# Optimization experiments

Measured on AMD Instinct MI355X. Metric: run time of the kernel, lower is better.

## Reference

```python
import jax, jax.numpy as jnp
import numpy as np

B, T, D, H, DEPTH, FF, NC = 512, 150, 256, 8, 6, 1024, 4
HD = D // H  # head dim = 32


def setup_inputs() -> dict:
    key = jax.random.key(0)
    ks = iter(jax.random.split(key, 64))
    n = lambda shape, s=0.02: jax.random.normal(next(ks), shape, jnp.float32) * s
    return dict(
        token_types=jax.random.randint(next(ks), (B, T), 0, 4, jnp.int32),
        decision_ids=jax.random.randint(next(ks), (B, T), 0, NC, jnp.int32),
        action_vals=jax.random.normal(next(ks), (B, T, 1), jnp.float32),
        dis_vals=jax.random.normal(next(ks), (B, T, 10), jnp.float32),
        v_vals=jax.random.normal(next(ks), (B, T, 3), jnp.float32),
        action_W=n((1, D), 0.5), action_b=n((D,)),
        dis_W=n((10, D), 0.2), dis_b=n((D,)),
        v_W=n((3, D), 0.3), v_b=n((D,)),
        decision_table=n((NC, D)),
        pos_embed=n((1, T + 1, D)), cls_token=n((1, 1, D)),
        qkv_W=n((DEPTH, D, 3 * D), 0.05), qkv_b=jnp.zeros((DEPTH, 3 * D), jnp.float32),
        out_W=n((DEPTH, D, D), 0.05), out_b=jnp.zeros((DEPTH, D), jnp.float32),
        ln1_g=jnp.ones((DEPTH, D), jnp.float32), ln1_b=jnp.zeros((DEPTH, D), jnp.float32),
        ln2_g=jnp.ones((DEPTH, D), jnp.float32), ln2_b=jnp.zeros((DEPTH, D), jnp.float32),
        ffn1_W=n((DEPTH, D, FF), 0.05), ffn1_b=jnp.zeros((DEPTH, FF), jnp.float32),
        ffn2_W=n((DEPTH, FF, D), 0.05), ffn2_b=jnp.zeros((DEPTH, D), jnp.float32),
        dec_ln_g=jnp.ones((D,), jnp.float32), dec_ln_b=jnp.zeros((D,), jnp.float32),
        dec_W=n((D, NC), 0.05), dec_b=jnp.zeros((NC,), jnp.float32),
        act_ln_g=jnp.ones((D,), jnp.float32), act_ln_b=jnp.zeros((D,), jnp.float32),
        act_W=n((D, 1), 0.05), act_b=jnpp if False else jnp.zeros((1,), jnp.float32),
    )


def _ln(x, g, b):
    # PyTorch LayerNorm: eps=1e-5, biased variance
    m = jnp.mean(x, axis=-1, keepdims=True)
    v = jnp.mean(jnp.square(x - m), axis=-1, keepdims=True)
    return (x - m) * jax.lax.rsqrt(v + 1e-5) * g + b


def reference(token_types, decision_ids, action_vals, dis_vals, v_vals,
              action_W, action_b, dis_W, dis_b, v_W, v_b, decision_table,
              pos_embed, cls_token, qkv_W, qkv_b, out_W, out_b,
              ln1_g, ln1_b, ln2_g, ln2_b, ffn1_W, ffn1_b, ffn2_W, ffn2_b,
              dec_ln_g, dec_ln_b, dec_W, dec_b, act_ln_g, act_ln_b, act_W, act_b):
    # --- batched type-dispatched token embedding (replaces the per-token python loop) ---
    a_emb = action_vals @ action_W + action_b                     # [B,T,D] type 'A'
    s_emb = dis_vals @ dis_W + dis_b + v_vals @ v_W + v_b         # [B,T,D] type 'S'
    d_emb = decision_table[decision_ids]                          # [B,T,D] type 'D'
    t = token_types[..., None]
    x = jnp.where(t == 0, a_emb, jnp.where(t == 1, s_emb, jnp.where(t == 2, d_emb, 0.0)))
    # --- prepend CLS, add positional embedding ---
    x = jnp.concatenate([jnp.broadcast_to(cls_token, (x.shape[0], 1, D)), x], axis=1)
    S = x.shape[1]
    x = x + pos_embed[:, :S, :]
    # --- post-norm TransformerEncoder (PyTorch default: ReLU FFN, norm_first=False, eval/no dropout) ---
    scale = 1.0 / np.sqrt(HD).astype(np.float32)
    for i in range(DEPTH):
        qkv = x @ qkv_W[i] + qkv_b[i]                             # [B,S,3D]
        q, k, v = jnp.split(qkv, 3, axis=-1)
        q = q.reshape(-1, S, H, HD)
        k = k.reshape(-1, S, H, HD)
        v = v.reshape(-1, S, H, HD)
        att = jax.nn.softmax(jnp.einsum('bqhd,bkhd->bhqk', q, k) * scale, axis=-1)
        o = jnp.einsum('bhqk,bkhd->bqhd', att, v).reshape(-1, S, D)
        x = _ln(x + o @ out_W[i] + out_b[i], ln1_g[i], ln1_b[i])
        ff = jax.nn.relu(x @ ffn1_W[i] + ffn1_b[i]) @ ffn2_W[i] + ffn2_b[i]
        x = _ln(x + ff, ln2_g[i], ln2_b[i])
    cls = x[:, 0, :]
    decision_logits = _ln(cls, dec_ln_g, dec_ln_b) @ dec_W + dec_b   # [B,4]
    action_pred = _ln(cls, act_ln_g, act_ln_b) @ act_W + act_b       # [B,1]
    return (decision_logits, action_pred)
```

## Files before the change

kernel.cpp:

```cpp
#include <hip/hip_runtime.h>
#include <hip/hip_bf16.h>

typedef __hip_bfloat16 bf16;
typedef unsigned short u16;
typedef __attribute__((ext_vector_type(8))) short s16x8;
typedef __attribute__((ext_vector_type(4))) float f32x4;

#define B_ 512
#define T_ 150
#define S_ 151
#define D_ 256
#define H_ 8
#define HD_ 32
#define FF_ 1024
#define NC_ 4
#define DEPTH_ 6
#define MTOT 77312
#define MT128 (MTOT / 128)
#define MT64 (MTOT / 64)

#define XOFF 0
#define C1OFF (MTOT * D_)
#define C2OFF (C1OFF + MTOT * FF_)
#define WSELEMS (C2OFF + MTOT * D_)

#define QKVT_OFF 0
#define OUTT_OFF (QKVT_OFF + DEPTH_ * D_ * 768)
#define FFN1T_OFF (OUTT_OFF + DEPTH_ * D_ * D_)
#define FFN2T_OFF (FFN1T_OFF + DEPTH_ * D_ * FF_)
#define WTELEMS (FFN2T_OFF + DEPTH_ * FF_ * D_)

__device__ __align__(16) u16 g_ws[WSELEMS];
__device__ __align__(16) u16 g_wt[WTELEMS];
__device__ int g_f32flag;

__device__ __forceinline__ float ldf(const void* p, size_t i, int f) {
  return f ? ((const float*)p)[i] : __bfloat162float(((const bf16*)p)[i]);
}
__device__ __forceinline__ float b2f(u16 u) {
  union { unsigned int i; float f; } v; v.i = ((unsigned int)u) << 16; return v.f;
}
__device__ __forceinline__ u16 f2b(float x) {
  bf16 h = __float2bfloat16(x);
  return *reinterpret_cast<u16*>(&h);
}

typedef __attribute__((address_space(3))) void lds_void;
typedef const __attribute__((address_space(1))) void glob_void;
__device__ __forceinline__ void gload_lds16(const u16* g, u16* l) {
  __builtin_amdgcn_global_load_lds((glob_void*)g, (lds_void*)l, 16, 0, 0);
}

#define PROBE_N 38656
__global__ __launch_bounds__(256) void probe_kernel(const void* pe)
{
  const u16* w = (const u16*)pe;
  int susp = 0, zeroEven = 0;
  for (int k = threadIdx.x; k < PROBE_N; k += 256) {
    u16 u = w[k];
    int ex = (u >> 7) & 0xFF;
    if (ex >= 141) susp++;
    if ((k & 1) == 0 && (u & 0x7FFF) == 0) zeroEven++;
  }
  __shared__ int s_susp, s_zero;
  if (threadIdx.x == 0) { s_susp = 0; s_zero = 0; }
  __syncthreads();
  atomicAdd(&s_susp, susp);
  atomicAdd(&s_zero, zeroEven);
  __syncthreads();
  if (threadIdx.x == 0)
    g_f32flag = (s_susp > 0 || s_zero >= ((PROBE_N / 2) * 9) / 10) ? 1 : 0;
}

__global__ __launch_bounds__(256) void wtrans_kernel(const void* src, int dstOff,
                                                     int K, int N, int total)
{
  const int f = g_f32flag;
  int idx = blockIdx.x * 256 + threadIdx.x;
  if (idx >= total) return;
  int kn = K * N;
  int l = idx / kn;
  int r = idx - l * kn;
  int k = r / N;
  int n = r - k * N;
  g_wt[dstOff + (size_t)l * kn + (size_t)n * K + k] = f2b(ldf(src, idx, f));
}

__global__ __launch_bounds__(256) void embed_kernel(
    const int* __restrict__ tt, const int* __restrict__ dids,
    const void* av, const void* dv, const void* vv,
    const void* aW, const void* ab, const void* dW, const void* db,
    const void* vW, const void* vb, const void* table, const void* pos,
    const void* cls)
{
  const int f = g_f32flag;
  u16* x = g_ws + XOFF;
  int row = blockIdx.x;
  int d = threadIdx.x;
  int b = row / S_;
  int s = row - b * S_;
  float val;
  if (s == 0) {
    val = ldf(cls, d, f);
  } else {
    int t = s - 1;
    int idx = b * T_ + t;
    int ty = tt[idx];
    if (ty == 0) {
      val = ldf(av, idx, f) * ldf(aW, d, f) + ldf(ab, d, f);
    } else if (ty == 1) {
      float acc = ldf(db, d, f) + ldf(vb, d, f);
#pragma unroll
      for (int i = 0; i < 10; i++) acc += ldf(dv, (size_t)idx * 10 + i, f) * ldf(dW, i * D_ + d, f);
#pragma unroll
      for (int i = 0; i < 3; i++) acc += ldf(vv, (size_t)idx * 3 + i, f) * ldf(vW, i * D_ + d, f);
      val = acc;
    } else if (ty == 2) {
      int did = dids[idx] & (NC_ - 1);
      val = ldf(table, (size_t)did * D_ + d, f);
    } else {
      val = 0.f;
    }
  }
  val += ldf(pos, s * D_ + d, f);
  x[(size_t)row * D_ + d] = f2b(val);
}

__global__ __launch_bounds__(256, 3) void gemm_mfma(
    int aOff, int wtOff, const void* bias, size_t bOff,
    int cOff, int N, int K, int relu, int NB)
{
  const int f = g_f32flag;
  const u16* A = g_ws + aOff;
  const u16* Bt = g_wt + wtOff;
  u16* C = g_ws + cOff;
  __shared__ __align__(16) u16 sm[16384];
  const int tid = threadIdx.x;

  int gblk = blockIdx.x;
  int bm, bn;
  {
    const int full = (MT128 / 8) * 8;
    if (gblk < NB * full) {
      int per = NB * 8;
      int grp = gblk / per, rem = gblk % per;
      bm = grp * 8 + (rem & 7);
      bn = rem >> 3;
    } else {
      int id = gblk - NB * full;
      bm = full + id / NB;
      bn = id % NB;
    }
  }

  const int lane = tid & 63, wid = tid >> 6;
  const int wm = (wid >> 1) * 64, wn = (wid & 1) * 64;
  const int frow = lane & 15, quad = lane >> 4;

  const int rg = lane >> 3;
  const int ck = ((lane & 7) ^ rg) * 8;
  const u16* Ag[4]; const u16* Bg[4];
  u16 *Asl[4], *Bsl[4];
#pragma unroll
  for (int p = 0; p < 4; p++) {
    int grp = wid * 4 + p;
    int row = grp * 8 + rg;
    Ag[p] = A + (size_t)(bm * 128 + row) * K + ck;
    Bg[p] = Bt + (size_t)(bn * 128 + row) * K + ck;
    Asl[p] = &sm[grp * 512];
    Bsl[p] = &sm[8192 + grp * 512];
  }

  f32x4 acc[4][4] = {};

  for (int kt = 0; kt < K; kt += 64) {
    if (kt) __syncthreads();
#pragma unroll
    for (int p = 0; p < 4; p++) {
      gload_lds16(Ag[p] + kt, Asl[p]);
      gload_lds16(Bg[p] + kt, Bsl[p]);
    }
    __syncthreads();
#pragma unroll
    for (int s = 0; s < 2; s++) {
      s16x8 af[4], bfr[4];
      const int cfr = ((s * 4 + quad) ^ (frow & 7)) * 8;
#pragma unroll
      for (int t = 0; t < 4; t++) {
        af[t]  = *(const s16x8*)&sm[(wm + t * 16 + frow) * 64 + cfr];
        bfr[t] = *(const s16x8*)&sm[8192 + (wn + t * 16 + frow) * 64 + cfr];
      }
#pragma unroll
      for (int mt = 0; mt < 4; mt++)
#pragma unroll
        for (int nt = 0; nt < 4; nt++)
          acc[mt][nt] = __builtin_amdgcn_mfma_f32_16x16x32_bf16(af[mt], bfr[nt], acc[mt][nt], 0, 0, 0);
    }
  }

  float bv[4];
#pragma unroll
  for (int nt = 0; nt < 4; nt++)
    bv[nt] = ldf(bias, bOff + (size_t)(bn * 128 + wn + nt * 16 + frow), f);
  __syncthreads();
#pragma unroll
  for (int p = 0; p < 2; p++) {
    if ((wid >> 1) == p) {
#pragma unroll
      for (int mt = 0; mt < 4; mt++)
#pragma unroll
        for (int nt = 0; nt < 4; nt++)
#pragma unroll
          for (int r = 0; r < 4; r++) {
            int rl = (wm & 63) + mt * 16 + quad * 4 + r;
            float v = acc[mt][nt][r] + bv[nt];
            if (relu) v = fmaxf(v, 0.f);
            sm[rl * 136 + wn + nt * 16 + frow] = f2b(v);
          }
    }
    __syncthreads();
    {
      int rl = tid >> 2;
      int cq = (tid & 3) * 32;
      size_t gb = (size_t)(bm * 128 + p * 64 + rl) * N + bn * 128 + cq;
#pragma unroll
      for (int j = 0; j < 4; j++)
        *(s16x8*)(C + gb + j * 8) = *(const s16x8*)&sm[rl * 136 + cq + j * 8];
    }
    __syncthreads();
  }
}

__global__ __launch_bounds__(256, 4) void gemm_ln(
    int aOff, int wtOff, const void* bias, size_t bOff,
    const void* lng, const void* lnb, size_t lnOff, int K)
{
  const int f = g_f32flag;
  const u16* A = g_ws + aOff;
  const u16* Bt = g_wt + wtOff;
  __shared__ __align__(16) u16 sm[20480];
  const int tid = threadIdx.x;
  const int bm = blockIdx.x;
  const int lane = tid & 63, wid = tid >> 6;
  const int wn = wid * 64;
  const int frow = lane & 15, quad = lane >> 4;
  const int rg = lane >> 3;
  const int ck = ((lane & 7) ^ rg) * 8;

  const u16* Ag[2]; u16* Asl[2];
  const u16* Bg[8]; u16* Bsl[8];
#pragma unroll
  for (int p = 0; p < 2; p++) {
    int grp = wid * 2 + p;
    Ag[p] = A + (size_t)(bm * 64 + grp * 8 + rg) * K + ck;
    Asl[p] = &sm[grp * 512];
  }
#pragma unroll
  for (int p = 0; p < 8; p++) {
    int grp = wid * 8 + p;
    Bg[p] = Bt + (size_t)(grp * 8 + rg) * K + ck;
    Bsl[p] = &sm[4096 + grp * 512];
  }

  f32x4 acc[4][4] = {};

  for (int kt = 0; kt < K; kt += 64) {
    if (kt) __syncthreads();
#pragma unroll
    for (int p = 0; p < 2; p++) gload_lds16(Ag[p] + kt, Asl[p]);
#pragma unroll
    for (int p = 0; p < 8; p++) gload_lds16(Bg[p] + kt, Bsl[p]);
    __syncthreads();
#pragma unroll
    for (int s = 0; s < 2; s++) {
      s16x8 af[4], bfr[4];
      const int cfr = ((s * 4 + quad) ^ (frow & 7)) * 8;
#pragma unroll
      for (int t = 0; t < 4; t++) {
        af[t]  = *(const s16x8*)&sm[(t * 16 + frow) * 64 + cfr];
        bfr[t] = *(const s16x8*)&sm[4096 + (wn + t * 16 + frow) * 64 + cfr];
      }
#pragma unroll
      for (int mt = 0; mt < 4; mt++)
#pragma unroll
        for (int nt = 0; nt < 4; nt++)
          acc[mt][nt] = __builtin_amdgcn_mfma_f32_16x16x32_bf16(af[mt], bfr[nt], acc[mt][nt], 0, 0, 0);
    }
  }

  float bv[4];
#pragma unroll
  for (int nt = 0; nt < 4; nt++)
    bv[nt] = ldf(bias, bOff + (size_t)(wn + nt * 16 + frow), f);
  __syncthreads();
#pragma unroll
  for (int mt = 0; mt < 4; mt++)
#pragma unroll
    for (int nt = 0; nt < 4; nt++)
#pragma unroll
      for (int r = 0; r < 4; r++) {
        int row = mt * 16 + quad * 4 + r;
        int col = wn + nt * 16 + frow;
        sm[row * 264 + col] = f2b(acc[mt][nt][r] + bv[nt]);
      }
  __syncthreads();
  {
    int rl = tid >> 2;
    int cq = (tid & 3) * 64;
    size_t rowg = (size_t)bm * 64 + rl;
    float s1 = 0.f, s2 = 0.f;
#pragma unroll
    for (int j = 0; j < 8; j++) {
      s16x8 yv = *(const s16x8*)&sm[rl * 264 + cq + j * 8];
      s16x8 xv = *(const s16x8*)(g_ws + XOFF + rowg * 256 + cq + j * 8);
#pragma unroll
      for (int e = 0; e < 8; e++) {
        float v = b2f((u16)yv[e]) + b2f((u16)xv[e]);
        s1 += v; s2 += v * v;
      }
    }
    s1 += __shfl_xor(s1, 1, 64); s2 += __shfl_xor(s2, 1, 64);
    s1 += __shfl_xor(s1, 2, 64); s2 += __shfl_xor(s2, 2, 64);
    float mean = s1 * (1.f / 256.f);
    float var = s2 * (1.f / 256.f) - mean * mean;
    float rs = rsqrtf(var + 1e-5f);
#pragma unroll
    for (int j = 0; j < 8; j++) {
      s16x8 yv = *(const s16x8*)&sm[rl * 264 + cq + j * 8];
      s16x8 xv = *(const s16x8*)(g_ws + XOFF + rowg * 256 + cq + j * 8);
      s16x8 ov;
#pragma unroll
      for (int e = 0; e < 8; e++) {
        float v = b2f((u16)yv[e]) + b2f((u16)xv[e]);
        int col = cq + j * 8 + e;
        ov[e] = (short)f2b((v - mean) * rs * ldf(lng, lnOff + col, f) + ldf(lnb, lnOff + col, f));
      }
      *(s16x8*)(g_ws + XOFF + rowg * 256 + cq + j * 8) = ov;
    }
  }
}

#define SP 160
#define KLD 32
#define VLD 170
#define PLDS 42

__global__ __launch_bounds__(320) void attn_kernel()
{
  const u16* qkv = g_ws + C1OFF;
  u16* o = g_ws + C2OFF;
  __shared__ __align__(16) u16 Ks[SP * KLD];
  __shared__ __align__(16) u16 Vt[HD_ * VLD];
  __shared__ __align__(16) u16 Ps[5][16 * PLDS];
  int bh = blockIdx.x;
  int b = bh >> 3, h = bh & 7;
  int tid = threadIdx.x;
  int lane = tid & 63, wid = tid >> 6;
  const u16* base = qkv + (size_t)b * S_ * 768;

  {
    const int jrow = lane >> 2;
    const int dsw = (((lane & 3) ^ ((lane >> 3) & 3)) * 8);
#pragma unroll
    for (int p = 0; p < 2; p++) {
      int g = wid * 2 + p;
      int j = g * 16 + jrow;
      gload_lds16(base + (size_t)j * 768 + 256 + h * 32 + dsw, &Ks[g * 512]);
    }
  }
  for (int g = tid; g < SP * 4; g += 320) {
    int j = g >> 2, d0 = (g & 3) * 8;
    s16x8 vv = {0, 0, 0, 0, 0, 0, 0, 0};
    if (j < S_) vv = *(const s16x8*)(base + (size_t)j * 768 + 512 + h * 32 + d0);
#pragma unroll
    for (int i = 0; i < 8; i++) Vt[(d0 + i) * VLD + j] = (u16)vv[i];
  }
  __syncthreads();

  const int frow = lane & 15;
  const int quad = lane >> 4;
  const int fk = quad * 8;
  const float scale = 0.17677669529663687f;
  u16* Pw = &Ps[wid][0];

  for (int round = 0; round < 2; round++) {
    int mt = round * 5 + wid;
    int qrow = mt * 16 + frow;
    s16x8 aq = {0, 0, 0, 0, 0, 0, 0, 0};
    if (qrow < S_) aq = *(const s16x8*)(base + (size_t)qrow * 768 + h * 32 + fk);
    f32x4 sacc[10];
#pragma unroll
    for (int nt = 0; nt < 10; nt++) {
      s16x8 bk = *(const s16x8*)&Ks[(nt * 16 + frow) * KLD
                                    + ((quad ^ ((frow >> 1) & 3)) * 8)];
      f32x4 z = {0.f, 0.f, 0.f, 0.f};
      sacc[nt] = __builtin_amdgcn_mfma_f32_16x16x32_bf16(aq, bk, z, 0, 0, 0);
    }
#pragma unroll
    for (int nt = 0; nt < 10; nt++) {
      int colg = nt * 16 + frow;
      float msk = (colg < S_) ? 1.f : 0.f;
#pragma unroll
      for (int r = 0; r < 4; r++)
        sacc[nt][r] = msk ? sacc[nt][r] * scale : -1e30f;
    }
    float inv[4];
#pragma unroll
    for (int r = 0; r < 4; r++) {
      float mx = -1e30f;
#pragma unroll
      for (int nt = 0; nt < 10; nt++) mx = fmaxf(mx, sacc[nt][r]);
#pragma unroll
      for (int m = 1; m < 16; m <<= 1) mx = fmaxf(mx, __shfl_xor(mx, m, 64));
      float sm2 = 0.f;
#pragma unroll
      for (int nt = 0; nt < 10; nt++) {
        float p = __expf(sacc[nt][r] - mx);
        sacc[nt][r] = p;
        sm2 += p;
      }
#pragma unroll
      for (int m = 1; m < 16; m <<= 1) sm2 += __shfl_xor(sm2, m, 64);
      inv[r] = 1.f / sm2;
    }
    f32x4 oacc[2] = {};
#pragma unroll
    for (int ks = 0; ks < 5; ks++) {
#pragma unroll
      for (int h2 = 0; h2 < 2; h2++) {
        int nt = ks * 2 + h2;
#pragma unroll
        for (int r = 0; r < 4; r++)
          Pw[(quad * 4 + r) * PLDS + h2 * 16 + frow] = f2b(sacc[nt][r]);
      }
      s16x8 ap = *(const s16x8*)&Pw[frow * PLDS + fk];
#pragma unroll
      for (int nt2 = 0; nt2 < 2; nt2++) {
        s16x8 bv = *(const s16x8*)&Vt[(nt2 * 16 + frow) * VLD + ks * 32 + fk];
        oacc[nt2] = __builtin_amdgcn_mfma_f32_16x16x32_bf16(ap, bv, oacc[nt2], 0, 0, 0);
      }
    }
#pragma unroll
    for (int nt2 = 0; nt2 < 2; nt2++)
#pragma unroll
      for (int r = 0; r < 4; r++) {
        int rowg = mt * 16 + quad * 4 + r;
        if (rowg < S_)
          o[(size_t)(b * S_ + rowg) * D_ + h * 32 + nt2 * 16 + frow] = f2b(oacc[nt2][r] * inv[r]);
      }
  }
}

__global__ __launch_bounds__(256) void head_kernel(
    const void* dg, const void* dbt, const void* dW, const void* dbias,
    const void* ag, const void* abt, const void* aW, const void* abias,
    void* out)
{
  const int f = g_f32flag;
  const u16* x = g_ws + XOFF;
  int bg = blockIdx.x;
  int tid = threadIdx.x;
  float c = b2f(x[(size_t)bg * S_ * D_ + tid]);
  float s1 = c, s2 = c * c;
#pragma unroll
  for (int off = 32; off > 0; off >>= 1) {
    s1 += __shfl_down(s1, off, 64);
    s2 += __shfl_down(s2, off, 64);
  }
  __shared__ float ws1[4], ws2[4], stats[2];
  __shared__ float lnD[256], lnA[256];
  int wid = tid >> 6, lane = tid & 63;
  if (lane == 0) { ws1[wid] = s1; ws2[wid] = s2; }
  __syncthreads();
  if (tid == 0) {
    float t1 = ws1[0] + ws1[1] + ws1[2] + ws1[3];
    float t2 = ws2[0] + ws2[1] + ws2[2] + ws2[3];
    float mean = t1 * (1.f / 256.f);
    float var = t2 * (1.f / 256.f) - mean * mean;
    stats[0] = mean;
    stats[1] = rsqrtf(var + 1e-5f);
  }
  __syncthreads();
  float n = (c - stats[0]) * stats[1];
  lnD[tid] = n * ldf(dg, tid, f) + ldf(dbt, tid, f);
  lnA[tid] = n * ldf(ag, tid, f) + ldf(abt, tid, f);
  __syncthreads();
  if (tid < NC_) {
    float acc = ldf(dbias, tid, f);
    for (int k = 0; k < D_; k++) acc += lnD[k] * ldf(dW, k * NC_ + tid, f);
    if (f) ((float*)out)[bg * NC_ + tid] = acc;
    else   ((bf16*)out)[bg * NC_ + tid] = __float2bfloat16(acc);
  } else if (tid == 8) {
    float acc = ldf(abias, 0, f);
    for (int k = 0; k < D_; k++) acc += lnA[k] * ldf(aW, k, f);
    if (f) ((float*)out)[B_ * NC_ + bg] = acc;
    else   ((bf16*)out)[B_ * NC_ + bg] = __float2bfloat16(acc);
  }
}

extern "C" void kernel_launch(void* const* d_in, const int* in_sizes, int n_in,
                              void* d_out, int out_size, void* d_ws, size_t ws_size,
                              hipStream_t stream)
{
  (void)in_sizes; (void)out_size; (void)d_ws; (void)ws_size;
  if (n_in < 34) return;
  const int* token_types  = (const int*)d_in[0];
  const int* decision_ids = (const int*)d_in[1];

  probe_kernel<<<1, 256, 0, stream>>>(d_in[12]);

  wtrans_kernel<<<(DEPTH_ * D_ * 768 + 255) / 256, 256, 0, stream>>>(
      d_in[14], QKVT_OFF, D_, 768, DEPTH_ * D_ * 768);
  wtrans_kernel<<<(DEPTH_ * D_ * D_ + 255) / 256, 256, 0, stream>>>(
      d_in[16], OUTT_OFF, D_, D_, DEPTH_ * D_ * D_);
  wtrans_kernel<<<(DEPTH_ * D_ * FF_ + 255) / 256, 256, 0, stream>>>(
      d_in[22], FFN1T_OFF, D_, FF_, DEPTH_ * D_ * FF_);
  wtrans_kernel<<<(DEPTH_ * FF_ * D_ + 255) / 256, 256, 0, stream>>>(
      d_in[24], FFN2T_OFF, FF_, D_, DEPTH_ * FF_ * D_);

  embed_kernel<<<MTOT, 256, 0, stream>>>(token_types, decision_ids,
      d_in[2], d_in[3], d_in[4], d_in[5], d_in[6], d_in[7], d_in[8],
      d_in[9], d_in[10], d_in[11], d_in[12], d_in[13]);

  for (int i = 0; i < DEPTH_; i++) {
    gemm_mfma<<<6 * MT128, 256, 0, stream>>>(XOFF,
        QKVT_OFF + i * D_ * 768, d_in[15], (size_t)i * 768, C1OFF, 768, D_, 0, 6);
    attn_kernel<<<B_ * H_, 320, 0, stream>>>();
    gemm_ln<<<MT64, 256, 0, stream>>>(C2OFF,
        OUTT_OFF + i * D_ * D_, d_in[17], (size_t)i * D_,
        d_in[18], d_in[19], (size_t)i * D_, D_);
    gemm_mfma<<<8 * MT128, 256, 0, stream>>>(XOFF,
        FFN1T_OFF + i * D_ * FF_, d_in[23], (size_t)i * FF_, C1OFF, FF_, D_, 1, 8);
    gemm_ln<<<MT64, 256, 0, stream>>>(C1OFF,
        FFN2T_OFF + i * FF_ * D_, d_in[25], (size_t)i * D_,
        d_in[20], d_in[21], (size_t)i * D_, FF_);
  }
  head_kernel<<<B_, 256, 0, stream>>>(d_in[26], d_in[27], d_in[28], d_in[29],
      d_in[30], d_in[31], d_in[32], d_in[33], d_out);
}
```

Baseline: 2.616 ms.

## Double-buffer LDS tiles in gemm_ln and preload residual rows into registers

Splits gemm_ln's LDS into two halves so the global-to-LDS loads for the next K step are issued while MFMAs run on the current step, with one barrier per iteration. It also loads the residual x rows into registers once, before the epilogue, instead of reading them from global memory twice during the LayerNorm. Doubling shared memory and lowering launch bounds from 4 to 2 blocks per CU cuts occupancy, which may offset the overlap gain.

```diff
diff --git a/kernel.cpp b/kernel.cpp
--- a/kernel.cpp
+++ b/kernel.cpp
@@ -231,14 +231,16 @@
   }
 }
 
-__global__ __launch_bounds__(256, 4) void gemm_ln(
+#define LNHALF 20480
+
+__global__ __launch_bounds__(256, 2) void gemm_ln(
     int aOff, int wtOff, const void* bias, size_t bOff,
     const void* lng, const void* lnb, size_t lnOff, int K)
 {
   const int f = g_f32flag;
   const u16* A = g_ws + aOff;
   const u16* Bt = g_wt + wtOff;
-  __shared__ __align__(16) u16 sm[20480];
+  __shared__ __align__(16) u16 sm[2 * LNHALF];
   const int tid = threadIdx.x;
   const int bm = blockIdx.x;
   const int lane = tid & 63, wid = tid >> 6;
@@ -263,22 +265,32 @@
   }
 
   f32x4 acc[4][4] = {};
-
-  for (int kt = 0; kt < K; kt += 64) {
-    if (kt) __syncthreads();
-#pragma unroll
-    for (int p = 0; p < 2; p++) gload_lds16(Ag[p] + kt, Asl[p]);
-#pragma unroll
-    for (int p = 0; p < 8; p++) gload_lds16(Bg[p] + kt, Bsl[p]);
-    __syncthreads();
+  const int nsteps = K >> 6;
+
+#pragma unroll
+  for (int p = 0; p < 2; p++) gload_lds16(Ag[p], Asl[p]);
+#pragma unroll
+  for (int p = 0; p < 8; p++) gload_lds16(Bg[p], Bsl[p]);
+  __syncthreads();
+
+  for (int t = 0; t < nsteps; t++) {
+    const int cur = (t & 1) * LNHALF;
+    if (t + 1 < nsteps) {
+      const int nxt = ((t + 1) & 1) * LNHALF;
+      const int kt = (t + 1) << 6;
+#pragma unroll
+      for (int p = 0; p < 2; p++) gload_lds16(Ag[p] + kt, Asl[p] + nxt);
+#pragma unroll
+      for (int p = 0; p < 8; p++) gload_lds16(Bg[p] + kt, Bsl[p] + nxt);
+    }
 #pragma unroll
     for (int s = 0; s < 2; s++) {
       s16x8 af[4], bfr[4];
       const int cfr = ((s * 4 + quad) ^ (frow & 7)) * 8;
 #pragma unroll
-      for (int t = 0; t < 4; t++) {
-        af[t]  = *(const s16x8*)&sm[(t * 16 + frow) * 64 + cfr];
-        bfr[t] = *(const s16x8*)&sm[4096 + (wn + t * 16 + frow) * 64 + cfr];
+      for (int ti = 0; ti < 4; ti++) {
+        af[ti]  = *(const s16x8*)&sm[cur + (ti * 16 + frow) * 64 + cfr];
+        bfr[ti] = *(const s16x8*)&sm[cur + 4096 + (wn + ti * 16 + frow) * 64 + cfr];
       }
 #pragma unroll
       for (int mt = 0; mt < 4; mt++)
@@ -286,13 +298,21 @@
         for (int nt = 0; nt < 4; nt++)
           acc[mt][nt] = __builtin_amdgcn_mfma_f32_16x16x32_bf16(af[mt], bfr[nt], acc[mt][nt], 0, 0, 0);
     }
-  }
+    __syncthreads();
+  }
+
+  const int rl = tid >> 2;
+  const int cq = (tid & 3) * 64;
+  const size_t rowg = (size_t)bm * 64 + rl;
+  s16x8 xr[8];
+#pragma unroll
+  for (int j = 0; j < 8; j++)
+    xr[j] = *(const s16x8*)(g_ws + XOFF + rowg * 256 + cq + j * 8);
 
   float bv[4];
 #pragma unroll
   for (int nt = 0; nt < 4; nt++)
     bv[nt] = ldf(bias, bOff + (size_t)(wn + nt * 16 + frow), f);
-  __syncthreads();
 #pragma unroll
   for (int mt = 0; mt < 4; mt++)
 #pragma unroll
@@ -305,17 +325,13 @@
       }
   __syncthreads();
   {
-    int rl = tid >> 2;
-    int cq = (tid & 3) * 64;
-    size_t rowg = (size_t)bm * 64 + rl;
     float s1 = 0.f, s2 = 0.f;
 #pragma unroll
     for (int j = 0; j < 8; j++) {
       s16x8 yv = *(const s16x8*)&sm[rl * 264 + cq + j * 8];
-      s16x8 xv = *(const s16x8*)(g_ws + XOFF + rowg * 256 + cq + j * 8);
 #pragma unroll
       for (int e = 0; e < 8; e++) {
-        float v = b2f((u16)yv[e]) + b2f((u16)xv[e]);
+        float v = b2f((u16)yv[e]) + b2f((u16)xr[j][e]);
         s1 += v; s2 += v * v;
       }
     }
@@ -327,11 +343,10 @@
 #pragma unroll
     for (int j = 0; j < 8; j++) {
       s16x8 yv = *(const s16x8*)&sm[rl * 264 + cq + j * 8];
-      s16x8 xv = *(const s16x8*)(g_ws + XOFF + rowg * 256 + cq + j * 8);
       s16x8 ov;
 #pragma unroll
       for (int e = 0; e < 8; e++) {
-        float v = b2f((u16)yv[e]) + b2f((u16)xv[e]);
+        float v = b2f((u16)yv[e]) + b2f((u16)xr[j][e]);
         int col = cq + j * 8 + e;
         ov[e] = (short)f2b((v - mean) * rs * ldf(lng, lnOff + col, f) + ldf(lnb, lnOff + col, f));
       }
```

New measurement: 2.532 ms. 3.2% less time.
